# Kernel tuning notes

Measured on AMD Instinct MI355X. Metric: run time of the kernel, lower is better.

Reference implementation:

```python
import jax, jax.numpy as jnp
import numpy as np

N_FREQS = 6  # PositionEmbedding N_freqs when embedding=='pe'

def _pe(x):
    freqs = (2.0 ** jnp.arange(N_FREQS)).astype(x.dtype)
    fx = x * freqs  # [B,Q,N_FREQS]
    sc = jnp.stack([jnp.sin(fx), jnp.cos(fx)], axis=-1).reshape(fx.shape[0], fx.shape[1], 2 * N_FREQS)
    return jnp.concatenate([x, sc], axis=-1)

def _mlp(h, W1, b1, W2, b2, W3, b3):
    h = jax.nn.relu(h @ W1 + b1)
    h = jax.nn.relu(h @ W2 + b2)
    return h @ W3 + b3

def setup_inputs() -> dict:
    key = jax.random.key(0)
    B, Q, N, D, H = 4, 65536, 8192, 16, 128
    ks = jax.random.split(key, 6)
    coord = jax.random.uniform(ks[0], (B, Q, 1), minval=-1.0, maxval=1.0, dtype=jnp.float32)
    latent = jax.random.normal(ks[1], (B, N, D), dtype=jnp.float32)
    in_dim = (1 + 2 * N_FREQS) + 3 * D  # pe(rel_coord) ++ unfolded feat = 13 + 48 = 61
    def init(k, shp, fan):
        return (jax.random.normal(k, shp, dtype=jnp.float32) / np.float32(np.sqrt(fan)))
    W1 = init(ks[2], (in_dim, H), in_dim); b1 = jnp.zeros((H,), jnp.float32)
    W2 = init(ks[3], (H, H), H);          b2 = jnp.zeros((H,), jnp.float32)
    W3 = init(ks[4], (H, 1), H);          b3 = jnp.zeros((1,), jnp.float32)
    return dict(coord=coord, latent=latent, W1=W1, b1=b1, W2=W2, b2=b2, W3=W3, b3=b3)

def reference(coord, latent, W1, b1, W2, b2, W3, b3):
    B, Q, _ = coord.shape
    N = latent.shape[1]
    # feat_unfold: concat shifted-prev / self / shifted-next along feature dim -> [B,N,3D]
    prev = jnp.concatenate([latent[:, :1], latent[:, :-1]], axis=1)
    nxt = jnp.concatenate([latent[:, 1:], latent[:, -1:]], axis=1)
    feat = jnp.concatenate([prev, latent, nxt], axis=-1)
    # make_coord grid: cell centers in [-1,1]
    grid = (-1.0 + (2.0 * jnp.arange(N, dtype=coord.dtype) + 1.0) / N)
    rx = 1.0 / N           # 2/num_latents/2
    eps_shift = 1e-6
    preds, areas = [], []
    for vx in (-2.0, 0.0):  # eval path vx_lst
        c = jnp.clip(coord + vx * rx + eps_shift, -1.0 + 1e-6, 1.0 - 1e-6)
        idx = jnp.clip(jnp.searchsorted(grid, c[..., 0]), 0, N - 1)  # [B,Q]
        q_coord = grid[idx][..., None]                               # [B,Q,1]
        q_feat = jnp.take_along_axis(feat, idx[..., None], axis=1)   # [B,Q,3D]
        rel = (coord - q_coord) * N                                  # scaled rel coord
        area = jnp.abs(rel[..., 0]) + 1e-9                           # [B,Q]
        inp = jnp.concatenate([_pe(rel), q_feat], axis=-1)           # [B,Q,61]
        preds.append(_mlp(inp, W1, b1, W2, b2, W3, b3))              # [B,Q,1]
        areas.append(area)
    tot = areas[0] + areas[1]
    # local_ensemble: swap areas before weighting
    ret = preds[0] * (areas[1] / tot)[..., None] + preds[1] * (areas[0] / tot)[..., None]
    return ret
```

## Files before the change

### kernel.cpp

```cpp
#include <hip/hip_runtime.h>
#include <hip/hip_bf16.h>

typedef short s8v __attribute__((ext_vector_type(8)));
typedef float f4v __attribute__((ext_vector_type(4)));
typedef unsigned u4v __attribute__((ext_vector_type(4)));

__device__ __forceinline__ unsigned short f2bf(float x) {
  unsigned u = __builtin_bit_cast(unsigned, x);
  u += 0x7fffu + ((u >> 16) & 1u);
  return (unsigned short)(u >> 16);
}
#if __has_builtin(__builtin_amdgcn_cvt_pk_bf16_f32)
__device__ __forceinline__ unsigned pk2(float a, float b) {
  return __builtin_bit_cast(unsigned, __builtin_amdgcn_cvt_pk_bf16_f32(a, b));
}
#else
__device__ __forceinline__ unsigned pk2(float a, float b) {
  unsigned ua = __builtin_bit_cast(unsigned, a) + 0x8000u;
  unsigned ub = __builtin_bit_cast(unsigned, b) + 0x8000u;
  return __builtin_amdgcn_perm(ub, ua, 0x07060302u);
}
#endif

__device__ __forceinline__ void g2lds16(const void* g, void* l) {
  __builtin_amdgcn_global_load_lds(
      (const __attribute__((address_space(1))) unsigned*)g,
      (__attribute__((address_space(3))) unsigned*)l, 16, 0, 0);
}

__global__ void prep_kernel(const float* __restrict__ W1, const float* __restrict__ b1,
                            const float* __restrict__ W2, const float* __restrict__ latent,
                            unsigned short* __restrict__ wsW) {
  int e = blockIdx.x * 256 + threadIdx.x;
  if (e < 8192) {
    int frag = e >> 9, rem = e & 511, lane = rem >> 3, j = rem & 7;
    int h = frag >> 1, ks = frag & 1;
    int q4 = lane >> 4, l15 = lane & 15;
    int k = ks * 32 + q4 * 8 + j;
    int n = h * 16 + l15;
    float v;
    if (k < 13) v = W1[k * 128 + n];
    else if (k == 13) v = b1[n];
    else if (k < 16) v = 0.0f;
    else v = W1[(k - 3) * 128 + n];
    wsW[e] = f2bf(v);
  } else if (e < 24576) {
    int e2 = e - 8192;
    int frag = e2 >> 9, rem = e2 & 511, lane = rem >> 3, j = rem & 7;
    int h2 = frag >> 2, ks = frag & 3;
    int q4 = lane >> 4, l15 = lane & 15;
    int kd = (j < 4) ? (32 * ks + 4 * q4 + j) : (32 * ks + 16 + 4 * q4 + (j - 4));
    int n = h2 * 16 + l15;
    wsW[e] = f2bf(W2[kd * 128 + n]);
  } else {
    int i = e - 24576;
    wsW[e] = f2bf(latent[i]);
  }
}

__global__ __launch_bounds__(256, 2) void lisagon_main(
    const float* __restrict__ coord, const unsigned short* __restrict__ latbf,
    const unsigned short* __restrict__ W1f, const unsigned short* __restrict__ W2f,
    const float* __restrict__ b2, const float* __restrict__ W3,
    const float* __restrict__ b3, float* __restrict__ out) {
  __shared__ __align__(16) unsigned short A1[256 * 64];
  __shared__ __align__(16) unsigned short W2s[16384];
  __shared__ float AREA[256];
  __shared__ __align__(16) float BW[256];

  const int t = threadIdx.x;
  const int lane = t & 63, wv = t >> 6;
  const int l15 = lane & 15, q4 = lane >> 4;

#pragma unroll
  for (int it = 0; it < 8; it++) {
    int off = (it * 4 + wv) * 1024;
    g2lds16((const char*)W2f + off + lane * 16, (char*)W2s + off);
  }

  const s8v* W1fv = (const s8v*)W1f;
  s8v W1r[16];
#pragma unroll
  for (int i = 0; i < 16; i++) W1r[i] = W1fv[i * 64 + lane];

  if (t < 64) {
    ((float4*)BW)[t] = (t < 32) ? ((const float4*)b2)[t] : ((const float4*)W3)[t - 32];
  }

  {
    const int r = t;
    const int Rg = blockIdx.x * 256 + r;
    const int gq = Rg >> 1, p = Rg & 1;
    const float co = coord[gq];
    float c = (co + (p ? 0.0f : -0.000244140625f)) + 1e-6f;
    c = fminf(fmaxf(c, -1.0f + 1e-6f), 1.0f - 1e-6f);
    double u = ((double)c * 8192.0 + 8191.0) * 0.5;
    int idx = (int)ceil(u);
    idx = min(max(idx, 0), 8191);

    float qc = ((float)(2 * idx + 1) - 8192.0f) * (1.0f / 8192.0f);
    float rel = (co - qc) * 8192.0f;
    AREA[r] = fabsf(rel) + 1e-9f;

    uint4* A1v = (uint4*)A1;
    const uint4* latv = (const uint4*)(latbf + (size_t)(gq >> 16) * (8192 * 16));
    int rows3[3];
    rows3[0] = max(idx - 1, 0);
    rows3[1] = idx;
    rows3[2] = min(idx + 1, 8191);
    uint4 L0[3], L1[3];
#pragma unroll
    for (int s = 0; s < 3; s++) {
      L0[s] = latv[rows3[s] * 2 + 0];
      L1[s] = latv[rows3[s] * 2 + 1];
    }

    float v[16];
    v[0] = rel;
    float f = rel;
#pragma unroll
    for (int i = 0; i < 6; i++) {
      v[1 + 2 * i] = __sinf(f);
      v[2 + 2 * i] = __cosf(f);
      f = f + f;
    }
    v[13] = 1.0f;
    v[14] = 0.0f; v[15] = 0.0f;
#pragma unroll
    for (int ch = 0; ch < 2; ch++) {
      union { uint4 u4; unsigned us[4]; } pkv;
#pragma unroll
      for (int w = 0; w < 4; w++) pkv.us[w] = pk2(v[ch * 8 + 2 * w], v[ch * 8 + 2 * w + 1]);
      A1v[r * 8 + (ch ^ (r & 7))] = pkv.u4;
    }
#pragma unroll
    for (int s = 0; s < 3; s++) {
      int ch0 = 2 + 2 * s;
      A1v[r * 8 + (ch0 ^ (r & 7))]       = L0[s];
      A1v[r * 8 + ((ch0 + 1) ^ (r & 7))] = L1[s];
    }
  }
  __syncthreads();

  const s8v* W2sv = (const s8v*)W2s;
  const s8v* A1s  = (const s8v*)A1;
  const int rbase = wv * 64;

  s8v Bf[2][4];
#pragma unroll
  for (int ks = 0; ks < 2; ks++)
#pragma unroll
    for (int rt = 0; rt < 4; rt++) {
      int row = rbase + rt * 16 + l15;
      Bf[ks][rt] = A1s[row * 8 + ((ks * 4 + q4) ^ (row & 7))];
    }

  u4v bbv[4][4];
#pragma unroll
  for (int h = 0; h < 8; h++) {
    f4v a[4];
#pragma unroll
    for (int rt = 0; rt < 4; rt++) a[rt] = (f4v){0.f, 0.f, 0.f, 0.f};
#pragma unroll
    for (int ks = 0; ks < 2; ks++) {
#pragma unroll
      for (int rt = 0; rt < 4; rt++)
        a[rt] = __builtin_amdgcn_mfma_f32_16x16x32_bf16(W1r[h * 2 + ks], Bf[ks][rt],
                                                        a[rt], 0, 0, 0);
    }
#pragma unroll
    for (int rt = 0; rt < 4; rt++) {
      bbv[rt][h >> 1][2 * (h & 1)]     = pk2(fmaxf(a[rt][0], 0.f), fmaxf(a[rt][1], 0.f));
      bbv[rt][h >> 1][2 * (h & 1) + 1] = pk2(fmaxf(a[rt][2], 0.f), fmaxf(a[rt][3], 0.f));
    }
  }

  float s[4] = {0.f, 0.f, 0.f, 0.f};
#pragma unroll
  for (int h2 = 0; h2 < 8; h2++) {
    f4v a2[4];
    f4v b2v = ((const f4v*)BW)[h2 * 4 + q4];
#pragma unroll
    for (int rt = 0; rt < 4; rt++) a2[rt] = b2v;
#pragma unroll
    for (int ks = 0; ks < 4; ks++) {
      s8v Af = W2sv[(h2 * 4 + ks) * 64 + lane];
#pragma unroll
      for (int rt = 0; rt < 4; rt++)
        a2[rt] = __builtin_amdgcn_mfma_f32_16x16x32_bf16(
            Af, __builtin_bit_cast(s8v, bbv[rt][ks]), a2[rt], 0, 0, 0);
    }
    float4 w3v = ((const float4*)(BW + 128))[h2 * 4 + q4];
#pragma unroll
    for (int rt = 0; rt < 4; rt++) {
      s[rt] += fmaxf(a2[rt][0], 0.f) * w3v.x;
      s[rt] += fmaxf(a2[rt][1], 0.f) * w3v.y;
      s[rt] += fmaxf(a2[rt][2], 0.f) * w3v.z;
      s[rt] += fmaxf(a2[rt][3], 0.f) * w3v.w;
    }
  }

  const float b3s = b3[0];
#pragma unroll
  for (int rt = 0; rt < 4; rt++) {
    float pred = s[rt];
    pred += __shfl_xor(pred, 16, 64);
    pred += __shfl_xor(pred, 32, 64);
    pred += b3s;
    float other = __shfl_xor(pred, 1, 64);
    if (q4 == 0 && (l15 & 1) == 0) {
      int row0 = rbase + rt * 16 + l15;
      float a0 = AREA[row0], a1 = AREA[row0 + 1];
      float tot = a0 + a1;
      out[(blockIdx.x * 256 + row0) >> 1] = pred * (a1 / tot) + other * (a0 / tot);
    }
  }
}

extern "C" void kernel_launch(void* const* d_in, const int* in_sizes, int n_in,
                              void* d_out, int out_size, void* d_ws, size_t ws_size,
                              hipStream_t stream) {
  const float* coord  = (const float*)d_in[0];
  const float* latent = (const float*)d_in[1];
  const float* W1 = (const float*)d_in[2];
  const float* b1 = (const float*)d_in[3];
  const float* W2 = (const float*)d_in[4];
  const float* b2 = (const float*)d_in[5];
  const float* W3 = (const float*)d_in[6];
  const float* b3 = (const float*)d_in[7];
  float* out = (float*)d_out;
  unsigned short* wsW = (unsigned short*)d_ws;

  prep_kernel<<<2144, 256, 0, stream>>>(W1, b1, W2, latent, wsW);
  lisagon_main<<<2048, 256, 0, stream>>>(coord, wsW + 24576, wsW, wsW + 8192,
                                         b2, W3, b3, out);
}
```

Before: 99.88 us.

## Gather latent rows straight into MFMA fragments and drop the A1 LDS staging

Removes the 32KB shared-memory A1 tile. Each lane now loads its own 16-byte slice of the prev/self/next latent rows directly into the layer-1 B-operand registers, using the row index fetched with a wave shuffle. Only the positional-encoding part goes through a small per-wave LDS buffer, and the area values are also exchanged by shuffle. The block barrier moves to just before layer 2, so the asynchronous W2 load to LDS can overlap layer-1 compute. The cost is more scattered global gathers per lane and extra shuffles, in exchange for fewer LDS round-trips and a smaller LDS footprint.

New measurement: 97.24 us. 1.03x faster.

```diff
diff --git a/kernel.cpp b/kernel.cpp
--- a/kernel.cpp
+++ b/kernel.cpp
@@ -63,9 +63,8 @@
     const unsigned short* __restrict__ W1f, const unsigned short* __restrict__ W2f,
     const float* __restrict__ b2, const float* __restrict__ W3,
     const float* __restrict__ b3, float* __restrict__ out) {
-  __shared__ __align__(16) unsigned short A1[256 * 64];
   __shared__ __align__(16) unsigned short W2s[16384];
-  __shared__ float AREA[256];
+  __shared__ __align__(16) unsigned PE[2][256][4];
   __shared__ __align__(16) float BW[256];
 
   const int t = threadIdx.x;
@@ -77,44 +76,28 @@
     int off = (it * 4 + wv) * 1024;
     g2lds16((const char*)W2f + off + lane * 16, (char*)W2s + off);
   }
-
+  if (t < 64) {
+    ((float4*)BW)[t] = (t < 32) ? ((const float4*)b2)[t] : ((const float4*)W3)[t - 32];
+  }
   const s8v* W1fv = (const s8v*)W1f;
   s8v W1r[16];
 #pragma unroll
   for (int i = 0; i < 16; i++) W1r[i] = W1fv[i * 64 + lane];
 
-  if (t < 64) {
-    ((float4*)BW)[t] = (t < 32) ? ((const float4*)b2)[t] : ((const float4*)W3)[t - 32];
-  }
-
+  int idx;
+  float area;
   {
-    const int r = t;
-    const int Rg = blockIdx.x * 256 + r;
+    const int Rg = blockIdx.x * 256 + t;
     const int gq = Rg >> 1, p = Rg & 1;
     const float co = coord[gq];
     float c = (co + (p ? 0.0f : -0.000244140625f)) + 1e-6f;
     c = fminf(fmaxf(c, -1.0f + 1e-6f), 1.0f - 1e-6f);
     double u = ((double)c * 8192.0 + 8191.0) * 0.5;
-    int idx = (int)ceil(u);
+    idx = (int)ceil(u);
     idx = min(max(idx, 0), 8191);
-
     float qc = ((float)(2 * idx + 1) - 8192.0f) * (1.0f / 8192.0f);
     float rel = (co - qc) * 8192.0f;
-    AREA[r] = fabsf(rel) + 1e-9f;
-
-    uint4* A1v = (uint4*)A1;
-    const uint4* latv = (const uint4*)(latbf + (size_t)(gq >> 16) * (8192 * 16));
-    int rows3[3];
-    rows3[0] = max(idx - 1, 0);
-    rows3[1] = idx;
-    rows3[2] = min(idx + 1, 8191);
-    uint4 L0[3], L1[3];
-#pragma unroll
-    for (int s = 0; s < 3; s++) {
-      L0[s] = latv[rows3[s] * 2 + 0];
-      L1[s] = latv[rows3[s] * 2 + 1];
-    }
-
+    area = fabsf(rel) + 1e-9f;
     float v[16];
     v[0] = rel;
     float f = rel;
@@ -126,34 +109,34 @@
     }
     v[13] = 1.0f;
     v[14] = 0.0f; v[15] = 0.0f;
-#pragma unroll
-    for (int ch = 0; ch < 2; ch++) {
-      union { uint4 u4; unsigned us[4]; } pkv;
-#pragma unroll
-      for (int w = 0; w < 4; w++) pkv.us[w] = pk2(v[ch * 8 + 2 * w], v[ch * 8 + 2 * w + 1]);
-      A1v[r * 8 + (ch ^ (r & 7))] = pkv.u4;
-    }
-#pragma unroll
-    for (int s = 0; s < 3; s++) {
-      int ch0 = 2 + 2 * s;
-      A1v[r * 8 + (ch0 ^ (r & 7))]       = L0[s];
-      A1v[r * 8 + ((ch0 + 1) ^ (r & 7))] = L1[s];
-    }
-  }
-  __syncthreads();
-
-  const s8v* W2sv = (const s8v*)W2s;
-  const s8v* A1s  = (const s8v*)A1;
+    uint4 q0, q1;
+    q0.x = pk2(v[0], v[1]);   q0.y = pk2(v[2], v[3]);
+    q0.z = pk2(v[4], v[5]);   q0.w = pk2(v[6], v[7]);
+    q1.x = pk2(v[8], v[9]);   q1.y = pk2(v[10], v[11]);
+    q1.z = pk2(v[12], v[13]); q1.w = pk2(v[14], v[15]);
+    ((uint4*)PE[0])[t] = q0;
+    ((uint4*)PE[1])[t] = q1;
+  }
+
+  const size_t bbase = (size_t)(blockIdx.x >> 9) * (8192 * 16);
+  const uint4* latv4 = (const uint4*)(latbf + bbase);
   const int rbase = wv * 64;
-
   s8v Bf[2][4];
 #pragma unroll
-  for (int ks = 0; ks < 2; ks++)
-#pragma unroll
-    for (int rt = 0; rt < 4; rt++) {
-      int row = rbase + rt * 16 + l15;
-      Bf[ks][rt] = A1s[row * 8 + ((ks * 4 + q4) ^ (row & 7))];
-    }
+  for (int rt = 0; rt < 4; rt++) {
+    int srcl = rt * 16 + l15;
+    int sidx = __shfl(idx, srcl, 64);
+    int rp = max(sidx - 1, 0), rn = min(sidx + 1, 8191);
+    int c = q4 & 1;
+    uint4 g0 = latv4[rp * 2 + c];
+    uint4 g1 = latv4[(q4 < 2 ? sidx : rn) * 2 + c];
+    uint4 pe = ((const uint4*)PE[c])[rbase + srcl];
+    uint4 b0;
+    b0.x = q4 < 2 ? pe.x : g0.x;  b0.y = q4 < 2 ? pe.y : g0.y;
+    b0.z = q4 < 2 ? pe.z : g0.z;  b0.w = q4 < 2 ? pe.w : g0.w;
+    Bf[0][rt] = __builtin_bit_cast(s8v, b0);
+    Bf[1][rt] = __builtin_bit_cast(s8v, g1);
+  }
 
   u4v bbv[4][4];
 #pragma unroll
@@ -175,6 +158,9 @@
     }
   }
 
+  __syncthreads();
+
+  const s8v* W2sv = (const s8v*)W2s;
   float s[4] = {0.f, 0.f, 0.f, 0.f};
 #pragma unroll
   for (int h2 = 0; h2 < 8; h2++) {
@@ -208,9 +194,10 @@
     pred += __shfl_xor(pred, 32, 64);
     pred += b3s;
     float other = __shfl_xor(pred, 1, 64);
+    float a0 = __shfl(area, rt * 16 + l15, 64);
+    float a1 = __shfl(area, rt * 16 + l15 + 1, 64);
     if (q4 == 0 && (l15 & 1) == 0) {
       int row0 = rbase + rt * 16 + l15;
-      float a0 = AREA[row0], a1 = AREA[row0 + 1];
       float tot = a0 + a1;
       out[(blockIdx.x * 256 + row0) >> 1] = pred * (a1 / tot) + other * (a0 / tot);
     }
```
